# Optimization experiments

Measured on AMD Instinct MI355X. Metric: run time of the kernel, lower is better.

Reference implementation:

```python
import jax, jax.numpy as jnp
import numpy as np

NUM_HEADS = 12
DIM_HEADS = 8  # number of sub-heads the depth is split into


def _split_into_heads(x, num_heads, dim_heads):
    # x: [B, S, E] -> [B, H, D, S, sub]  (D = dim_heads, sub = E/(H*D))
    B, S, E = x.shape
    depth = E // num_heads
    sub = depth // dim_heads
    x = x.reshape(B, S, num_heads, dim_heads, sub)
    return x.transpose(0, 2, 3, 1, 4)  # [B, H, D, S, sub]


def setup_inputs() -> dict:
    key = jax.random.key(0)
    ks = jax.random.split(key, 8)
    B, S, E = 2, 1024, 768
    sc_in = 1.0 / np.sqrt(E)
    return {
        "k": jax.random.normal(ks[0], (B, S, E), dtype=jnp.float32),
        "q": jax.random.normal(ks[1], (B, S, E), dtype=jnp.float32),
        "Wq_w": jax.random.normal(ks[2], (E, E), dtype=jnp.float32) * sc_in,
        "Wq_b": jax.random.normal(ks[3], (E,), dtype=jnp.float32) * 0.01,
        "Wk_w": jax.random.normal(ks[4], (E, E), dtype=jnp.float32) * sc_in,
        "Wk_b": jax.random.normal(ks[5], (E,), dtype=jnp.float32) * 0.01,
        "lin_w": jax.random.normal(ks[6], (DIM_HEADS,), dtype=jnp.float32) * (1.0 / np.sqrt(DIM_HEADS)),
        "lin_b": jax.random.normal(ks[7], (), dtype=jnp.float32) * 0.01,
    }


def reference(k, q, Wq_w, Wq_b, Wk_w, Wk_b, lin_w, lin_b):
    # Linear projections (torch Linear: x @ W^T + b)
    qp = q @ Wq_w.T + Wq_b  # [B, S, E]
    kp = k @ Wk_w.T + Wk_b  # [B, S, E]

    qh = _split_into_heads(qp, NUM_HEADS, DIM_HEADS)  # [B, H, D, S, sub]
    kh = _split_into_heads(kp, NUM_HEADS, DIM_HEADS)  # [B, H, D, S, sub]
    sub = kh.shape[-1]
    scale = 1.0 / np.sqrt(sub).astype(np.float32)

    # Original: scores[b,h,d,i,j] = (qh @ kh^T)/sqrt(sub), permute to [b,h,i,j,d],
    # dropout (identity at eval), then Linear(D,1).squeeze(-1).
    out = jnp.einsum("bhdis,bhdjs,d->bhij", qh, kh, lin_w) * scale + lin_b
    return out  # [B, H, S, S]
```

## Files before the change

kernel.cpp:

```cpp
#include <hip/hip_runtime.h>
#include <hip/hip_bf16.h>

#define S_ 1024
#define E_ 768
#define H_ 12

typedef __bf16  bf16x8 __attribute__((ext_vector_type(8)));
typedef float   f32x4  __attribute__((ext_vector_type(4)));
typedef unsigned short u16x8 __attribute__((ext_vector_type(8)));
typedef unsigned short u16x4 __attribute__((ext_vector_type(4)));

__device__ __forceinline__ unsigned short f2bf(float f) {
    union { float f; unsigned u; } a; a.f = f;
    unsigned u = a.u;
    u += 0x7FFFu + ((u >> 16) & 1u);
    return (unsigned short)(u >> 16);
}

__device__ __forceinline__ u16x8 pack8(float4 a, float4 b) {
    u16x8 o;
    o[0] = f2bf(a.x); o[1] = f2bf(a.y); o[2] = f2bf(a.z); o[3] = f2bf(a.w);
    o[4] = f2bf(b.x); o[5] = f2bf(b.y); o[6] = f2bf(b.z); o[7] = f2bf(b.w);
    return o;
}

__device__ __forceinline__ bf16x8 ld_frag(const char* lbase, int row, int kk, int lane) {
    int cbyte = (kk * 64 + ((lane >> 4) * 16)) ^ ((row & 7) << 4);
    return *(const bf16x8*)(lbase + row * 128 + cbyte);
}

__global__ __launch_bounds__(256) void prep_w_kernel(
    const float* __restrict__ Wq, const float* __restrict__ bq,
    const float* __restrict__ Wk, const float* __restrict__ lin_w,
    unsigned short* __restrict__ Wqbf, unsigned short* __restrict__ Wkbf,
    float* __restrict__ bqs)
{
    const float invs = 0.35355339059327373f;
    int idx4 = blockIdx.x * 256 + threadIdx.x;
    int i = idx4 * 4;
    if (blockIdx.z == 0) {
        int n = i / E_;
        float w = lin_w[(n & 63) >> 3] * invs;
        float4 v = *(const float4*)(Wq + i);
        ushort4 o = make_ushort4(f2bf(v.x * w), f2bf(v.y * w), f2bf(v.z * w), f2bf(v.w * w));
        *(ushort4*)(Wqbf + i) = o;
        if (idx4 < E_) bqs[idx4] = bq[idx4] * (lin_w[(idx4 & 63) >> 3] * invs);
    } else {
        float4 v = *(const float4*)(Wk + i);
        ushort4 o = make_ushort4(f2bf(v.x), f2bf(v.y), f2bf(v.z), f2bf(v.w));
        *(ushort4*)(Wkbf + i) = o;
    }
}

__global__ __launch_bounds__(256) void proj_kernel(
    const float* __restrict__ q_in, const float* __restrict__ k_in,
    const unsigned short* __restrict__ Wqbf, const unsigned short* __restrict__ Wkbf,
    const float* __restrict__ bqs, const float* __restrict__ bk,
    unsigned short* __restrict__ qs, unsigned short* __restrict__ kp)
{
    __shared__ char lds[32768];

    int lid = blockIdx.x;
    int swz = (lid & 7) * 96 + (lid >> 3);
    int z  = swz / 384;
    int rem = swz - z * 384;
    int ty = rem / 12, tx = rem - ty * 12;
    int tm = ty * 64, tn = tx * 64;

    const float* X          = z ? k_in : q_in;
    const unsigned short* W = z ? Wkbf : Wqbf;
    const float* bias       = z ? bk   : bqs;
    unsigned short* P       = z ? kp   : qs;

    int tid = threadIdx.x, lane = tid & 63, wid = tid >> 6;
    int wn = wid >> 1, wm = wid & 1;

    int c0 = tid,        r0 = c0 >> 3, g0 = ((c0 & 7) ^ (r0 & 7)) * 8;
    int c1 = 256 + tid,  r1 = c1 >> 3, g1 = ((c1 & 7) ^ (r1 & 7)) * 8;

    const float* Xg          = X + (size_t)tm * E_;
    const unsigned short* Wg = W + (size_t)tn * E_;

    float4 xv0, xv1, xv2, xv3;
#define LOADX(kb) { \
    const float* xs0 = Xg + r0 * E_ + (kb) + g0; xv0 = *(const float4*)xs0; xv1 = *(const float4*)(xs0 + 4); \
    const float* xs1 = Xg + r1 * E_ + (kb) + g1; xv2 = *(const float4*)xs1; xv3 = *(const float4*)(xs1 + 4); }
#define WRITEX(buf) { \
    char* xb = lds + (buf) * 8192; \
    *(u16x8*)(xb + c0 * 16) = pack8(xv0, xv1); \
    *(u16x8*)(xb + c1 * 16) = pack8(xv2, xv3); }
#define STAGEW(kb, buf) { \
    char* wb = lds + 16384 + (buf) * 8192; \
    __builtin_amdgcn_global_load_lds( \
        (const __attribute__((address_space(1))) void*)(Wg + (size_t)r0 * E_ + (kb) + g0), \
        (__attribute__((address_space(3))) void*)(wb + c0 * 16), 16, 0, 0); \
    __builtin_amdgcn_global_load_lds( \
        (const __attribute__((address_space(1))) void*)(Wg + (size_t)r1 * E_ + (kb) + g1), \
        (__attribute__((address_space(3))) void*)(wb + c1 * 16), 16, 0, 0); }

    f32x4 acc[2][2];
#pragma unroll
    for (int nj = 0; nj < 2; ++nj) {
        int n0 = tn + wn * 32 + nj * 16 + ((lane >> 4) << 2);
        float4 b4 = *(const float4*)(bias + n0);
#pragma unroll
        for (int mi = 0; mi < 2; ++mi)
            acc[nj][mi] = f32x4{b4.x, b4.y, b4.z, b4.w};
    }

#define COMPSTEP(buf) { \
    const char* Xc = lds + (buf) * 8192; \
    const char* Wc = lds + 16384 + (buf) * 8192; \
    _Pragma("unroll") \
    for (int kk = 0; kk < 2; ++kk) { \
        bf16x8 a0 = ld_frag(Wc, wn * 32 + (lane & 15), kk, lane); \
        bf16x8 a1 = ld_frag(Wc, wn * 32 + 16 + (lane & 15), kk, lane); \
        bf16x8 b0 = ld_frag(Xc, wm * 32 + (lane & 15), kk, lane); \
        bf16x8 b1 = ld_frag(Xc, wm * 32 + 16 + (lane & 15), kk, lane); \
        acc[0][0] = __builtin_amdgcn_mfma_f32_16x16x32_bf16(a0, b0, acc[0][0], 0, 0, 0); \
        acc[0][1] = __builtin_amdgcn_mfma_f32_16x16x32_bf16(a0, b1, acc[0][1], 0, 0, 0); \
        acc[1][0] = __builtin_amdgcn_mfma_f32_16x16x32_bf16(a1, b0, acc[1][0], 0, 0, 0); \
        acc[1][1] = __builtin_amdgcn_mfma_f32_16x16x32_bf16(a1, b1, acc[1][1], 0, 0, 0); \
    } }

    STAGEW(0, 0);
    LOADX(0);
    WRITEX(0);
    __syncthreads();
    int cur = 0;
#pragma unroll 2
    for (int t = 0; t < 11; ++t) {
        STAGEW((t + 1) * 64, cur ^ 1);
        LOADX((t + 1) * 64);
        COMPSTEP(cur);
        WRITEX(cur ^ 1);
        __syncthreads();
        cur ^= 1;
    }
    COMPSTEP(cur);

#pragma unroll
    for (int nj = 0; nj < 2; ++nj)
#pragma unroll
        for (int mi = 0; mi < 2; ++mi) {
            int n0 = tn + wn * 32 + nj * 16 + ((lane >> 4) << 2);
            int m  = tm + wm * 32 + mi * 16 + (lane & 15);
            u16x4 pk;
            pk[0] = f2bf(acc[nj][mi][0]); pk[1] = f2bf(acc[nj][mi][1]);
            pk[2] = f2bf(acc[nj][mi][2]); pk[3] = f2bf(acc[nj][mi][3]);
            *(u16x4*)(P + (size_t)m * E_ + n0) = pk;
        }
#undef LOADX
#undef WRITEX
#undef STAGEW
#undef COMPSTEP
}

__global__ __launch_bounds__(256) void scores_kernel(
    const unsigned short* __restrict__ qs, const unsigned short* __restrict__ kp,
    const float* __restrict__ lin_b, float* __restrict__ out)
{
    __shared__ char lds[32768];

    int lid = blockIdx.x;
    int swz = (lid & 7) * 96 + (lid >> 3);
    int z   = swz >> 5;
    int rem = swz & 31;
    int iy  = rem >> 2, jx = rem & 3;
    int b = z / H_, h = z - b * H_;

    int tid = threadIdx.x, lane = tid & 63, wid = tid >> 6;
    int wj = wid >> 1, wi = wid & 1;
    int ti = iy * 128, tj = jx * 256;

    const unsigned short* Qg = qs + (size_t)(b * S_) * E_ + h * 64;
    const unsigned short* Kg = kp + (size_t)(b * S_) * E_ + h * 64;

#define STAGEK(jbase, buf) { \
    char* lb = lds + (buf) * 16384; \
    _Pragma("unroll") \
    for (int pass = 0; pass < 4; ++pass) { \
        int c = pass * 256 + tid; \
        int row = c >> 3, cbg = (c & 7) ^ (row & 7); \
        __builtin_amdgcn_global_load_lds( \
            (const __attribute__((address_space(1))) void*)(Kg + (size_t)((jbase) + row) * E_ + cbg * 8), \
            (__attribute__((address_space(3))) void*)(lb + c * 16), 16, 0, 0); \
    } }

    bf16x8 qf[2][4];
    int qrow = ti + wi * 64 + (lane & 15);
#pragma unroll
    for (int ni = 0; ni < 4; ++ni)
#pragma unroll
        for (int kk = 0; kk < 2; ++kk)
            qf[kk][ni] = *(const bf16x8*)(Qg + (size_t)(qrow + ni * 16) * E_ + kk * 32 + ((lane >> 4) * 8));

    float lb0 = lin_b[0];
    float* O = out + ((size_t)z << 20);

    STAGEK(tj, 0);
    __syncthreads();
    STAGEK(tj + 128, 1);

    f32x4 acc[4][4];

#pragma unroll
    for (int mj = 0; mj < 4; ++mj)
#pragma unroll
        for (int ni = 0; ni < 4; ++ni) acc[mj][ni] = f32x4{lb0, lb0, lb0, lb0};
#pragma unroll
    for (int kk = 0; kk < 2; ++kk) {
        bf16x8 a[4];
#pragma unroll
        for (int mj = 0; mj < 4; ++mj) a[mj] = ld_frag(lds, wj * 64 + mj * 16 + (lane & 15), kk, lane);
#pragma unroll
        for (int mj = 0; mj < 4; ++mj)
#pragma unroll
            for (int ni = 0; ni < 4; ++ni)
                acc[mj][ni] = __builtin_amdgcn_mfma_f32_16x16x32_bf16(a[mj], qf[kk][ni], acc[mj][ni], 0, 0, 0);
    }

    __syncthreads();

#pragma unroll
    for (int mj = 0; mj < 4; ++mj)
#pragma unroll
        for (int ni = 0; ni < 4; ++ni) {
            int i  = ti + wi * 64 + ni * 16 + (lane & 15);
            int j0 = tj + wj * 64 + mj * 16 + ((lane >> 4) << 2);
            *(f32x4*)(O + (size_t)i * S_ + j0) = acc[mj][ni];
        }

#pragma unroll
    for (int mj = 0; mj < 4; ++mj)
#pragma unroll
        for (int ni = 0; ni < 4; ++ni) acc[mj][ni] = f32x4{lb0, lb0, lb0, lb0};
#pragma unroll
    for (int kk = 0; kk < 2; ++kk) {
        bf16x8 a[4];
#pragma unroll
        for (int mj = 0; mj < 4; ++mj) a[mj] = ld_frag(lds + 16384, wj * 64 + mj * 16 + (lane & 15), kk, lane);
#pragma unroll
        for (int mj = 0; mj < 4; ++mj)
#pragma unroll
            for (int ni = 0; ni < 4; ++ni)
                acc[mj][ni] = __builtin_amdgcn_mfma_f32_16x16x32_bf16(a[mj], qf[kk][ni], acc[mj][ni], 0, 0, 0);
    }

#pragma unroll
    for (int mj = 0; mj < 4; ++mj)
#pragma unroll
        for (int ni = 0; ni < 4; ++ni) {
            int i  = ti + wi * 64 + ni * 16 + (lane & 15);
            int j0 = tj + 128 + wj * 64 + mj * 16 + ((lane >> 4) << 2);
            *(f32x4*)(O + (size_t)i * S_ + j0) = acc[mj][ni];
        }
#undef STAGEK
}

extern "C" void kernel_launch(void* const* d_in, const int* in_sizes, int n_in,
                              void* d_out, int out_size, void* d_ws, size_t ws_size,
                              hipStream_t stream)
{
    const float* k_in  = (const float*)d_in[0];
    const float* q_in  = (const float*)d_in[1];
    const float* Wq_w  = (const float*)d_in[2];
    const float* Wq_b  = (const float*)d_in[3];
    const float* Wk_w  = (const float*)d_in[4];
    const float* Wk_b  = (const float*)d_in[5];
    const float* lin_w = (const float*)d_in[6];
    const float* lin_b = (const float*)d_in[7];
    float* out = (float*)d_out;

    char* ws = (char*)d_ws;
    unsigned short* Wqbf = (unsigned short*)(ws + 0);
    unsigned short* Wkbf = (unsigned short*)(ws + 1179648);
    float*          bqs  = (float*)        (ws + 2359296);
    unsigned short* qsb  = (unsigned short*)(ws + 2362368);
    unsigned short* kpb  = (unsigned short*)(ws + 5508096);

    prep_w_kernel<<<dim3(576, 1, 2), dim3(256), 0, stream>>>(Wq_w, Wq_b, Wk_w, lin_w, Wqbf, Wkbf, bqs);
    proj_kernel<<<dim3(768), dim3(256), 0, stream>>>(q_in, k_in, Wqbf, Wkbf, bqs, Wk_b, qsb, kpb);
    scores_kernel<<<dim3(768), dim3(256), 0, stream>>>(qsb, kpb, lin_b, out);
}
```

Before: 45.34 us.

## Triple-buffer weight tiles in projection, load K directly to registers in scores

The projection GEMM now keeps three LDS buffers for the weight tile, prefetching two K-steps ahead, and uses explicit vmcnt/lgkmcnt waits with raw barriers in place of __syncthreads so loads can stay in flight across iterations. The scores kernel drops LDS staging and its barriers entirely and loads K fragments straight from global memory into registers per 128-column half. The prep kernel switches to a flat 1D grid. This aims to hide memory latency and remove synchronisation, but adds LDS use in proj and relies on hand-counted waitcnt values being correct.

```diff
diff --git a/kernel.cpp b/kernel.cpp
--- a/kernel.cpp
+++ b/kernel.cpp
@@ -30,25 +30,24 @@
 }
 
 __global__ __launch_bounds__(256) void prep_w_kernel(
-    const float* __restrict__ Wq, const float* __restrict__ bq,
-    const float* __restrict__ Wk, const float* __restrict__ lin_w,
+    const float* __restrict__ Wq, const float* __restrict__ Wk,
+    const float* __restrict__ bq, const float* __restrict__ lin_w,
     unsigned short* __restrict__ Wqbf, unsigned short* __restrict__ Wkbf,
     float* __restrict__ bqs)
 {
     const float invs = 0.35355339059327373f;
-    int idx4 = blockIdx.x * 256 + threadIdx.x;
-    int i = idx4 * 4;
-    if (blockIdx.z == 0) {
+    int u = blockIdx.x * 256 + threadIdx.x;
+    if (u < 147456) {
+        int i = u * 4;
         int n = i / E_;
         float w = lin_w[(n & 63) >> 3] * invs;
         float4 v = *(const float4*)(Wq + i);
-        ushort4 o = make_ushort4(f2bf(v.x * w), f2bf(v.y * w), f2bf(v.z * w), f2bf(v.w * w));
-        *(ushort4*)(Wqbf + i) = o;
-        if (idx4 < E_) bqs[idx4] = bq[idx4] * (lin_w[(idx4 & 63) >> 3] * invs);
+        *(ushort4*)(Wqbf + i) = make_ushort4(f2bf(v.x * w), f2bf(v.y * w), f2bf(v.z * w), f2bf(v.w * w));
+        if (u < E_) bqs[u] = bq[u] * (lin_w[(u & 63) >> 3] * invs);
     } else {
+        int i = (u - 147456) * 4;
         float4 v = *(const float4*)(Wk + i);
-        ushort4 o = make_ushort4(f2bf(v.x), f2bf(v.y), f2bf(v.z), f2bf(v.w));
-        *(ushort4*)(Wkbf + i) = o;
+        *(ushort4*)(Wkbf + i) = make_ushort4(f2bf(v.x), f2bf(v.y), f2bf(v.z), f2bf(v.w));
     }
 }
 
@@ -58,7 +57,7 @@
     const float* __restrict__ bqs, const float* __restrict__ bk,
     unsigned short* __restrict__ qs, unsigned short* __restrict__ kp)
 {
-    __shared__ char lds[32768];
+    __shared__ char lds[2 * 8192 + 3 * 8192];
 
     int lid = blockIdx.x;
     int swz = (lid & 7) * 96 + (lid >> 3);
@@ -81,7 +80,13 @@
     const float* Xg          = X + (size_t)tm * E_;
     const unsigned short* Wg = W + (size_t)tn * E_;
 
-    float4 xv0, xv1, xv2, xv3;
+#define GLL(src, dst) __builtin_amdgcn_global_load_lds( \
+        (const __attribute__((address_space(1))) void*)(src), \
+        (__attribute__((address_space(3))) void*)(dst), 16, 0, 0)
+#define GLLW(kb, buf) { \
+    char* wb = lds + 16384 + (buf) * 8192; \
+    GLL(Wg + (size_t)r0 * E_ + (kb) + g0, wb + c0 * 16); \
+    GLL(Wg + (size_t)r1 * E_ + (kb) + g1, wb + c1 * 16); }
 #define LOADX(kb) { \
     const float* xs0 = Xg + r0 * E_ + (kb) + g0; xv0 = *(const float4*)xs0; xv1 = *(const float4*)(xs0 + 4); \
     const float* xs1 = Xg + r1 * E_ + (kb) + g1; xv2 = *(const float4*)xs1; xv3 = *(const float4*)(xs1 + 4); }
@@ -89,14 +94,8 @@
     char* xb = lds + (buf) * 8192; \
     *(u16x8*)(xb + c0 * 16) = pack8(xv0, xv1); \
     *(u16x8*)(xb + c1 * 16) = pack8(xv2, xv3); }
-#define STAGEW(kb, buf) { \
-    char* wb = lds + 16384 + (buf) * 8192; \
-    __builtin_amdgcn_global_load_lds( \
-        (const __attribute__((address_space(1))) void*)(Wg + (size_t)r0 * E_ + (kb) + g0), \
-        (__attribute__((address_space(3))) void*)(wb + c0 * 16), 16, 0, 0); \
-    __builtin_amdgcn_global_load_lds( \
-        (const __attribute__((address_space(1))) void*)(Wg + (size_t)r1 * E_ + (kb) + g1), \
-        (__attribute__((address_space(3))) void*)(wb + c1 * 16), 16, 0, 0); }
+
+    float4 xv0, xv1, xv2, xv3;
 
     f32x4 acc[2][2];
 #pragma unroll
@@ -108,9 +107,9 @@
             acc[nj][mi] = f32x4{b4.x, b4.y, b4.z, b4.w};
     }
 
-#define COMPSTEP(buf) { \
-    const char* Xc = lds + (buf) * 8192; \
-    const char* Wc = lds + 16384 + (buf) * 8192; \
+#define COMPSTEP(xbuf, wbuf) { \
+    const char* Xc = lds + (xbuf) * 8192; \
+    const char* Wc = lds + 16384 + (wbuf) * 8192; \
     _Pragma("unroll") \
     for (int kk = 0; kk < 2; ++kk) { \
         bf16x8 a0 = ld_frag(Wc, wn * 32 + (lane & 15), kk, lane); \
@@ -123,21 +122,42 @@
         acc[1][1] = __builtin_amdgcn_mfma_f32_16x16x32_bf16(a1, b1, acc[1][1], 0, 0, 0); \
     } }
 
-    STAGEW(0, 0);
+    GLLW(0, 0);
     LOADX(0);
+    GLLW(64, 1);
     WRITEX(0);
-    __syncthreads();
-    int cur = 0;
-#pragma unroll 2
-    for (int t = 0; t < 11; ++t) {
-        STAGEW((t + 1) * 64, cur ^ 1);
+    asm volatile("s_waitcnt lgkmcnt(0)" ::: "memory");
+    __builtin_amdgcn_s_barrier();
+    __builtin_amdgcn_sched_barrier(0);
+
+    int xc = 0, wc = 0, wn2 = 2;
+    for (int t = 0; t < 10; ++t) {
         LOADX((t + 1) * 64);
-        COMPSTEP(cur);
-        WRITEX(cur ^ 1);
-        __syncthreads();
-        cur ^= 1;
-    }
-    COMPSTEP(cur);
+        GLLW((t + 2) * 64, wn2);
+        __builtin_amdgcn_sched_barrier(0);
+        asm volatile("s_waitcnt vmcnt(8)" ::: "memory");
+        __builtin_amdgcn_sched_barrier(0);
+        COMPSTEP(xc, wc);
+        WRITEX(xc ^ 1);
+        asm volatile("s_waitcnt lgkmcnt(0)" ::: "memory");
+        __builtin_amdgcn_s_barrier();
+        __builtin_amdgcn_sched_barrier(0);
+        xc ^= 1;
+        wc = wc == 2 ? 0 : wc + 1;
+        wn2 = wn2 == 2 ? 0 : wn2 + 1;
+    }
+    LOADX(11 * 64);
+    __builtin_amdgcn_sched_barrier(0);
+    asm volatile("s_waitcnt vmcnt(6)" ::: "memory");
+    __builtin_amdgcn_sched_barrier(0);
+    COMPSTEP(0, 1);
+    WRITEX(1);
+    asm volatile("s_waitcnt lgkmcnt(0)" ::: "memory");
+    __builtin_amdgcn_s_barrier();
+    __builtin_amdgcn_sched_barrier(0);
+    asm volatile("s_waitcnt vmcnt(0)" ::: "memory");
+    __builtin_amdgcn_sched_barrier(0);
+    COMPSTEP(1, 2);
 
 #pragma unroll
     for (int nj = 0; nj < 2; ++nj)
@@ -150,9 +170,10 @@
             pk[2] = f2bf(acc[nj][mi][2]); pk[3] = f2bf(acc[nj][mi][3]);
             *(u16x4*)(P + (size_t)m * E_ + n0) = pk;
         }
+#undef GLL
+#undef GLLW
 #undef LOADX
 #undef WRITEX
-#undef STAGEW
 #undef COMPSTEP
 }
 
@@ -160,8 +181,6 @@
     const unsigned short* __restrict__ qs, const unsigned short* __restrict__ kp,
     const float* __restrict__ lin_b, float* __restrict__ out)
 {
-    __shared__ char lds[32768];
-
     int lid = blockIdx.x;
     int swz = (lid & 7) * 96 + (lid >> 3);
     int z   = swz >> 5;
@@ -176,17 +195,6 @@
     const unsigned short* Qg = qs + (size_t)(b * S_) * E_ + h * 64;
     const unsigned short* Kg = kp + (size_t)(b * S_) * E_ + h * 64;
 
-#define STAGEK(jbase, buf) { \
-    char* lb = lds + (buf) * 16384; \
-    _Pragma("unroll") \
-    for (int pass = 0; pass < 4; ++pass) { \
-        int c = pass * 256 + tid; \
-        int row = c >> 3, cbg = (c & 7) ^ (row & 7); \
-        __builtin_amdgcn_global_load_lds( \
-            (const __attribute__((address_space(1))) void*)(Kg + (size_t)((jbase) + row) * E_ + cbg * 8), \
-            (__attribute__((address_space(3))) void*)(lb + c * 16), 16, 0, 0); \
-    } }
-
     bf16x8 qf[2][4];
     int qrow = ti + wi * 64 + (lane & 15);
 #pragma unroll
@@ -198,64 +206,39 @@
     float lb0 = lin_b[0];
     float* O = out + ((size_t)z << 20);
 
-    STAGEK(tj, 0);
-    __syncthreads();
-    STAGEK(tj + 128, 1);
-
-    f32x4 acc[4][4];
-
-#pragma unroll
-    for (int mj = 0; mj < 4; ++mj)
-#pragma unroll
-        for (int ni = 0; ni < 4; ++ni) acc[mj][ni] = f32x4{lb0, lb0, lb0, lb0};
-#pragma unroll
-    for (int kk = 0; kk < 2; ++kk) {
-        bf16x8 a[4];
-#pragma unroll
-        for (int mj = 0; mj < 4; ++mj) a[mj] = ld_frag(lds, wj * 64 + mj * 16 + (lane & 15), kk, lane);
+#pragma unroll
+    for (int sub = 0; sub < 2; ++sub) {
+        bf16x8 kf[2][4];
+        int krow = tj + sub * 128 + wj * 64 + (lane & 15);
 #pragma unroll
         for (int mj = 0; mj < 4; ++mj)
 #pragma unroll
-            for (int ni = 0; ni < 4; ++ni)
-                acc[mj][ni] = __builtin_amdgcn_mfma_f32_16x16x32_bf16(a[mj], qf[kk][ni], acc[mj][ni], 0, 0, 0);
-    }
-
-    __syncthreads();
-
-#pragma unroll
-    for (int mj = 0; mj < 4; ++mj)
-#pragma unroll
-        for (int ni = 0; ni < 4; ++ni) {
-            int i  = ti + wi * 64 + ni * 16 + (lane & 15);
-            int j0 = tj + wj * 64 + mj * 16 + ((lane >> 4) << 2);
-            *(f32x4*)(O + (size_t)i * S_ + j0) = acc[mj][ni];
-        }
-
-#pragma unroll
-    for (int mj = 0; mj < 4; ++mj)
-#pragma unroll
-        for (int ni = 0; ni < 4; ++ni) acc[mj][ni] = f32x4{lb0, lb0, lb0, lb0};
-#pragma unroll
-    for (int kk = 0; kk < 2; ++kk) {
-        bf16x8 a[4];
-#pragma unroll
-        for (int mj = 0; mj < 4; ++mj) a[mj] = ld_frag(lds + 16384, wj * 64 + mj * 16 + (lane & 15), kk, lane);
+            for (int kk = 0; kk < 2; ++kk)
+                kf[kk][mj] = *(const bf16x8*)(Kg + (size_t)(krow + mj * 16) * E_ + kk * 32 + ((lane >> 4) * 8));
+
+        f32x4 acc[4][4];
 #pragma unroll
         for (int mj = 0; mj < 4; ++mj)
 #pragma unroll
-            for (int ni = 0; ni < 4; ++ni)
-                acc[mj][ni] = __builtin_amdgcn_mfma_f32_16x16x32_bf16(a[mj], qf[kk][ni], acc[mj][ni], 0, 0, 0);
-    }
-
-#pragma unroll
-    for (int mj = 0; mj < 4; ++mj)
-#pragma unroll
-        for (int ni = 0; ni < 4; ++ni) {
-            int i  = ti + wi * 64 + ni * 16 + (lane & 15);
-            int j0 = tj + 128 + wj * 64 + mj * 16 + ((lane >> 4) << 2);
-            *(f32x4*)(O + (size_t)i * S_ + j0) = acc[mj][ni];
-        }
-#undef STAGEK
+            for (int ni = 0; ni < 4; ++ni) acc[mj][ni] = f32x4{lb0, lb0, lb0, lb0};
+
+#pragma unroll
+        for (int kk = 0; kk < 2; ++kk)
+#pragma unroll
+            for (int mj = 0; mj < 4; ++mj)
+#pragma unroll
+                for (int ni = 0; ni < 4; ++ni)
+                    acc[mj][ni] = __builtin_amdgcn_mfma_f32_16x16x32_bf16(kf[kk][mj], qf[kk][ni], acc[mj][ni], 0, 0, 0);
+
+#pragma unroll
+        for (int mj = 0; mj < 4; ++mj)
+#pragma unroll
+            for (int ni = 0; ni < 4; ++ni) {
+                int i  = ti + wi * 64 + ni * 16 + (lane & 15);
+                int j0 = tj + sub * 128 + wj * 64 + mj * 16 + ((lane >> 4) << 2);
+                *(f32x4*)(O + (size_t)i * S_ + j0) = acc[mj][ni];
+            }
+    }
 }
 
 extern "C" void kernel_launch(void* const* d_in, const int* in_sizes, int n_in,
@@ -279,7 +262,7 @@
     unsigned short* qsb  = (unsigned short*)(ws + 2362368);
     unsigned short* kpb  = (unsigned short*)(ws + 5508096);
 
-    prep_w_kernel<<<dim3(576, 1, 2), dim3(256), 0, stream>>>(Wq_w, Wq_b, Wk_w, lin_w, Wqbf, Wkbf, bqs);
+    prep_w_kernel<<<dim3(1152), dim3(256), 0, stream>>>(Wq_w, Wk_w, Wq_b, lin_w, Wqbf, Wkbf, bqs);
     proj_kernel<<<dim3(768), dim3(256), 0, stream>>>(q_in, k_in, Wqbf, Wkbf, bqs, Wk_b, qsb, kpb);
     scores_kernel<<<dim3(768), dim3(256), 0, stream>>>(qsb, kpb, lin_b, out);
 }
```

New measurement: 46.75 us. 1.03x slower.
